# Performance work log

Measured on AMD Instinct MI355X. Metric: run time of the kernel, lower is better.

## Reference

```python
import jax, jax.numpy as jnp
import numpy as np

N, C, A = 4096, 1000, 2048


def setup_inputs() -> dict:
    key = jax.random.key(0)
    k1, k2, k3, k4 = jax.random.split(key, 4)
    features = jax.random.normal(k1, (N, A), dtype=jnp.float32)
    labels = jax.random.randint(k2, (N,), 0, C, dtype=jnp.int64)
    cv_matrix = jax.random.uniform(k3, (N, A), dtype=jnp.float32)
    ratio = jnp.asarray(0.5, dtype=jnp.float32)
    weight = jax.random.normal(k4, (C, A), dtype=jnp.float32) * 0.02
    bias = jnp.zeros((C,), dtype=jnp.float32)
    return {"features": features, "labels": labels, "cv_matrix": cv_matrix,
            "ratio": ratio, "weight": weight, "bias": bias}


def reference(features, labels, cv_matrix, ratio, weight, bias):
    # logits = features @ W^T + b
    logits = features @ weight.T + bias  # [N, C]
    # sigma2[n,c] = ratio * sum_a (W[c,a] - W[y_n,a])^2 * cv[n,a]
    # Expand the square to avoid materializing the [N, C, A] tensor:
    #   = sum_a W[c,a]^2 cv - 2 sum_a W[c,a] (W[y,a] cv) + sum_a W[y,a]^2 cv
    Wy = weight[labels]                          # [N, A] gather of per-label rows
    t1 = cv_matrix @ (weight * weight).T         # [N, C]
    t2 = (cv_matrix * Wy) @ weight.T             # [N, C]
    t3 = jnp.sum(Wy * Wy * cv_matrix, axis=1, keepdims=True)  # [N, 1]
    sigma2 = ratio * (t1 - 2.0 * t2 + t3)        # [N, C]
    aug_logits = logits + 0.5 * sigma2
    # mean cross-entropy on augmented logits
    logp = jax.nn.log_softmax(aug_logits, axis=-1)
    nll = -jnp.take_along_axis(logp, labels[:, None], axis=1)[:, 0]
    loss = jnp.mean(nll)
    return loss, logits
```

## Files before the change

### kernel.cpp

```cpp
#include <hip/hip_runtime.h>
#include <hip/hip_bf16.h>

#define N_ROWS 4096
#define C_CLS  1000
#define C_PAD  1024
#define A_DIM  2048

typedef __attribute__((ext_vector_type(8))) short short8;
typedef __attribute__((ext_vector_type(4))) float f32x4;

__device__ __forceinline__ unsigned short f2bf(float x) {
    unsigned u = __float_as_uint(x);
    unsigned rounding = 0x7fffu + ((u >> 16) & 1u);
    return (unsigned short)((u + rounding) >> 16);
}

__device__ __forceinline__ float bf2f(unsigned short u) {
    return __uint_as_float((unsigned)u << 16);
}

__device__ __forceinline__ unsigned pack2(float a, float b) {
    return (unsigned)f2bf(a) | ((unsigned)f2bf(b) << 16);
}

__device__ __forceinline__ void gload16(unsigned short* lds, const unsigned short* g) {
    __builtin_amdgcn_global_load_lds(
        (const __attribute__((address_space(1))) unsigned int*)g,
        (__attribute__((address_space(3))) unsigned int*)lds,
        16, 0, 0);
}

__global__ __launch_bounds__(256) void prep_all(
        const float* __restrict__ F, const float* __restrict__ CV,
        const float* __restrict__ W, const int* __restrict__ labels,
        const float* __restrict__ ratio_p,
        unsigned short* __restrict__ Fb, unsigned short* __restrict__ Ub,
        unsigned short* __restrict__ Vb,
        unsigned short* __restrict__ Wb, unsigned short* __restrict__ W2b,
        float* __restrict__ t3c) {
    int bid = blockIdx.x;
    if (bid >= N_ROWS) {
        int t = (bid - N_ROWS) * 256 + threadIdx.x;
        int a8 = t * 8;
        int c = a8 >> 11;
        int a = a8 & (A_DIM - 1);
        float4 w0 = make_float4(0.f, 0.f, 0.f, 0.f);
        float4 w1 = make_float4(0.f, 0.f, 0.f, 0.f);
        if (c < C_CLS) {
            w0 = *(const float4*)(W + (size_t)c * A_DIM + a);
            w1 = *(const float4*)(W + (size_t)c * A_DIM + a + 4);
        }
        uint4 pw, pw2;
        pw.x  = pack2(w0.x, w0.y);  pw.y  = pack2(w0.z, w0.w);
        pw.z  = pack2(w1.x, w1.y);  pw.w  = pack2(w1.z, w1.w);
        pw2.x = pack2(w0.x*w0.x, w0.y*w0.y);  pw2.y = pack2(w0.z*w0.z, w0.w*w0.w);
        pw2.z = pack2(w1.x*w1.x, w1.y*w1.y);  pw2.w = pack2(w1.z*w1.z, w1.w*w1.w);
        *(uint4*)(Wb  + (size_t)a8) = pw;
        *(uint4*)(W2b + (size_t)a8) = pw2;
        return;
    }
    int n = bid;
    int y = labels[n];
    float ratio = ratio_p[0];
    float hr = 0.5f * ratio;
    const float* frow  = F  + (size_t)n * A_DIM;
    const float* cvrow = CV + (size_t)n * A_DIM;
    const float* wyrow = W  + (size_t)y * A_DIM;
    size_t obase = (size_t)n * A_DIM;

    int a = threadIdx.x * 8;
    float4 f0  = *(const float4*)(frow + a);
    float4 f1  = *(const float4*)(frow + a + 4);
    float4 c0  = *(const float4*)(cvrow + a);
    float4 c1  = *(const float4*)(cvrow + a + 4);
    float4 y0  = *(const float4*)(wyrow + a);
    float4 y1  = *(const float4*)(wyrow + a + 4);

    float s = y0.x*y0.x*c0.x + y0.y*y0.y*c0.y + y0.z*y0.z*c0.z + y0.w*y0.w*c0.w
            + y1.x*y1.x*c1.x + y1.y*y1.y*c1.y + y1.z*y1.z*c1.z + y1.w*y1.w*c1.w;

    uint4 pf, pu, pv;
    pf.x = pack2(f0.x, f0.y);  pf.y = pack2(f0.z, f0.w);
    pf.z = pack2(f1.x, f1.y);  pf.w = pack2(f1.z, f1.w);
    pu.x = pack2(f0.x - ratio*c0.x*y0.x, f0.y - ratio*c0.y*y0.y);
    pu.y = pack2(f0.z - ratio*c0.z*y0.z, f0.w - ratio*c0.w*y0.w);
    pu.z = pack2(f1.x - ratio*c1.x*y1.x, f1.y - ratio*c1.y*y1.y);
    pu.w = pack2(f1.z - ratio*c1.z*y1.z, f1.w - ratio*c1.w*y1.w);
    pv.x = pack2(hr*c0.x, hr*c0.y);  pv.y = pack2(hr*c0.z, hr*c0.w);
    pv.z = pack2(hr*c1.x, hr*c1.y);  pv.w = pack2(hr*c1.z, hr*c1.w);
    *(uint4*)(Fb + obase + a) = pf;
    *(uint4*)(Ub + obase + a) = pu;
    *(uint4*)(Vb + obase + a) = pv;

    for (int off = 32; off; off >>= 1) s += __shfl_down(s, off);
    __shared__ float wsum[4];
    int lane = threadIdx.x & 63, wid = threadIdx.x >> 6;
    if (lane == 0) wsum[wid] = s;
    __syncthreads();
    if (threadIdx.x == 0)
        t3c[n] = hr * (wsum[0] + wsum[1] + wsum[2] + wsum[3]);
}

#define BM 128
#define BN 64
#define BK 32
#define TILE_A (BM * BK)
#define TILE_B (BN * BK)
#define BUF_USH (3 * TILE_A + 2 * TILE_B)
#define NT (A_DIM / BK)

__global__ __launch_bounds__(256, 2) void gemm_fused(
        const unsigned short* __restrict__ Fb, const unsigned short* __restrict__ Ub,
        const unsigned short* __restrict__ Vb, const unsigned short* __restrict__ Wb,
        const unsigned short* __restrict__ W2b,
        const float* __restrict__ t3c, const float* __restrict__ bias,
        float* __restrict__ out_logits, unsigned short* __restrict__ aug) {
    __shared__ unsigned short lds[2 * BUF_USH];

    int bid = blockIdx.x;
    int xcd = bid & 7, idx = bid >> 3;
    int bn = (xcd << 1) | (idx & 1);
    int bm = idx >> 1;

    int tid = threadIdx.x;
    int lane = tid & 63, wid = tid >> 6;
    int wm = wid >> 1, wn = wid & 1;

    int srow = lane >> 2;
    int scs  = ((lane & 3) * 8) ^ (((srow >> 1) & 3) << 3);
    int r0 = wid * 16 + srow;
    size_t gA0 = (size_t)(bm * BM + r0) * A_DIM + scs;
    size_t gB0 = (size_t)(bn * BN + r0) * A_DIM + scs;
    const size_t gStep = (size_t)64 * A_DIM;
    int d0 = wid * 512;
    int d1 = 2048 + wid * 512;

    int fr = lane & 15;
    int kof = ((lane >> 4) * 8) ^ (((fr >> 1) & 3) << 3);
    int aoff = fr * BK + kof;

    f32x4 accL[4][2] = {};
    f32x4 accA[4][2] = {};

    {
        unsigned short* b = lds;
        gload16(b + 0*TILE_A + d0, Fb + gA0);
        gload16(b + 0*TILE_A + d1, Fb + gA0 + gStep);
        gload16(b + 1*TILE_A + d0, Ub + gA0);
        gload16(b + 1*TILE_A + d1, Ub + gA0 + gStep);
        gload16(b + 2*TILE_A + d0, Vb + gA0);
        gload16(b + 2*TILE_A + d1, Vb + gA0 + gStep);
        gload16(b + 3*TILE_A + d0,          Wb  + gB0);
        gload16(b + 3*TILE_A + TILE_B + d0, W2b + gB0);
    }
    __syncthreads();

    for (int t = 0; t < NT; t++) {
        unsigned short* cbuf = lds + (t & 1) * BUF_USH;
        if (t + 1 < NT) {
            unsigned short* b = lds + ((t + 1) & 1) * BUF_USH;
            size_t ka = gA0 + (size_t)(t + 1) * BK;
            size_t kb = gB0 + (size_t)(t + 1) * BK;
            gload16(b + 0*TILE_A + d0, Fb + ka);
            gload16(b + 0*TILE_A + d1, Fb + ka + gStep);
            gload16(b + 1*TILE_A + d0, Ub + ka);
            gload16(b + 1*TILE_A + d1, Ub + ka + gStep);
            gload16(b + 2*TILE_A + d0, Vb + ka);
            gload16(b + 2*TILE_A + d1, Vb + ka + gStep);
            gload16(b + 3*TILE_A + d0,          Wb  + kb);
            gload16(b + 3*TILE_A + TILE_B + d0, W2b + kb);
        }

        short8 aF[4], aU[4], aV[4], bWf[2], bW2f[2];
        #pragma unroll
        for (int m = 0; m < 4; m++) {
            int off = wm * 2048 + m * 512 + aoff;
            aF[m] = *(const short8*)(cbuf + 0*TILE_A + off);
            aU[m] = *(const short8*)(cbuf + 1*TILE_A + off);
            aV[m] = *(const short8*)(cbuf + 2*TILE_A + off);
        }
        #pragma unroll
        for (int n = 0; n < 2; n++) {
            int off = wn * 1024 + n * 512 + aoff;
            bWf[n]  = *(const short8*)(cbuf + 3*TILE_A + off);
            bW2f[n] = *(const short8*)(cbuf + 3*TILE_A + TILE_B + off);
        }
        #pragma unroll
        for (int m = 0; m < 4; m++)
            #pragma unroll
            for (int n = 0; n < 2; n++) {
                accL[m][n] = __builtin_amdgcn_mfma_f32_16x16x32_bf16(aF[m], bWf[n],  accL[m][n], 0, 0, 0);
                accA[m][n] = __builtin_amdgcn_mfma_f32_16x16x32_bf16(aU[m], bWf[n],  accA[m][n], 0, 0, 0);
                accA[m][n] = __builtin_amdgcn_mfma_f32_16x16x32_bf16(aV[m], bW2f[n], accA[m][n], 0, 0, 0);
            }

        __syncthreads();
    }

    #pragma unroll
    for (int n = 0; n < 2; n++) {
        int col = bn * BN + wn * 32 + n * 16 + fr;
        if (col < C_CLS) {
            float bv = bias[col];
            #pragma unroll
            for (int m = 0; m < 4; m++) {
                int rbase = bm * BM + wm * 64 + m * 16 + (lane >> 4) * 4;
                #pragma unroll
                for (int j = 0; j < 4; j++) {
                    int row = rbase + j;
                    out_logits[(size_t)row * C_CLS + col] = accL[m][n][j] + bv;
                    aug[(size_t)row * C_PAD + col] = f2bf(accA[m][n][j] + bv + t3c[row]);
                }
            }
        }
    }
}

__global__ __launch_bounds__(256) void softmax_nll(const unsigned short* __restrict__ aug,
                                                   const int* __restrict__ labels,
                                                   float* __restrict__ nll) {
    int n = blockIdx.x;
    const unsigned short* row = aug + (size_t)n * C_PAD;
    int tid = threadIdx.x;
    int lane = tid & 63, wid = tid >> 6;
    __shared__ float sm[4], ss[4];

    float v[8];
    bool act = tid < (C_CLS / 8);
    float mx = -1e30f;
    if (act) {
        short8 r8 = *(const short8*)(row + tid * 8);
        #pragma unroll
        for (int j = 0; j < 8; j++) {
            v[j] = bf2f((unsigned short)r8[j]);
            mx = fmaxf(mx, v[j]);
        }
    }
    for (int off = 32; off; off >>= 1) mx = fmaxf(mx, __shfl_down(mx, off));
    if (lane == 0) sm[wid] = mx;
    __syncthreads();
    mx = fmaxf(fmaxf(sm[0], sm[1]), fmaxf(sm[2], sm[3]));

    float s = 0.f;
    if (act) {
        #pragma unroll
        for (int j = 0; j < 8; j++) s += __expf(v[j] - mx);
    }
    for (int off = 32; off; off >>= 1) s += __shfl_down(s, off);
    if (lane == 0) ss[wid] = s;
    __syncthreads();
    if (tid == 0) {
        float tot = ss[0] + ss[1] + ss[2] + ss[3];
        nll[n] = logf(tot) + mx - bf2f(row[labels[n]]);
    }
}

__global__ __launch_bounds__(256) void final_reduce(const float* __restrict__ nll,
                                                    float* __restrict__ out_loss) {
    float s = 0.f;
    for (int i = threadIdx.x; i < N_ROWS; i += 256) s += nll[i];
    for (int off = 32; off; off >>= 1) s += __shfl_down(s, off);
    __shared__ float ss[4];
    int lane = threadIdx.x & 63, wid = threadIdx.x >> 6;
    if (lane == 0) ss[wid] = s;
    __syncthreads();
    if (threadIdx.x == 0)
        out_loss[0] = (ss[0] + ss[1] + ss[2] + ss[3]) / (float)N_ROWS;
}

extern "C" void kernel_launch(void* const* d_in, const int* in_sizes, int n_in,
                              void* d_out, int out_size, void* d_ws, size_t ws_size,
                              hipStream_t stream) {
    const float* features = (const float*)d_in[0];
    const int*   labels   = (const int*)d_in[1];
    const float* cv       = (const float*)d_in[2];
    const float* ratio    = (const float*)d_in[3];
    const float* weight   = (const float*)d_in[4];
    const float* bias     = (const float*)d_in[5];
    float* out = (float*)d_out;

    char* p = (char*)d_ws;
    unsigned short* Wb  = (unsigned short*)p; p += (size_t)C_PAD * A_DIM * 2;
    unsigned short* W2b = (unsigned short*)p; p += (size_t)C_PAD * A_DIM * 2;
    unsigned short* Fb  = (unsigned short*)p; p += (size_t)N_ROWS * A_DIM * 2;
    unsigned short* Ub  = (unsigned short*)p; p += (size_t)N_ROWS * A_DIM * 2;
    unsigned short* Vb  = (unsigned short*)p; p += (size_t)N_ROWS * A_DIM * 2;
    float* t3c = (float*)p; p += (size_t)N_ROWS * 4;
    unsigned short* aug = (unsigned short*)p; p += (size_t)N_ROWS * C_PAD * 2;
    float* nllb = (float*)p; p += (size_t)N_ROWS * 4;

    int wprep_blocks = (C_PAD * A_DIM / 8) / 256;
    prep_all<<<N_ROWS + wprep_blocks, 256, 0, stream>>>(
        features, cv, weight, labels, ratio, Fb, Ub, Vb, Wb, W2b, t3c);
    gemm_fused<<<(N_ROWS / BM) * (C_PAD / BN), 256, 0, stream>>>(
        Fb, Ub, Vb, Wb, W2b, t3c, bias, out + 1, aug);
    softmax_nll<<<N_ROWS, 256, 0, stream>>>(aug, labels, nllb);
    final_reduce<<<1, 256, 0, stream>>>(nllb, out);
}
```

Measured before the change: 214.8 us.

## Compute squared weights in-register and prefetch two K-tiles ahead with finer waits

Drops the precomputed W² bf16 buffer. The GEMM now squares the bf16 weight fragments in registers after they are loaded from LDS, which removes one global stream and one LDS tile per stage. The main loop is restructured so loads for tile t+2 are issued into the buffer just consumed, after a barrier placed following the LDS reads. Explicit vmcnt waits replace the full syncthreads, aiming to overlap global loads with MFMA work. The trade-offs are extra VALU work per iteration and slightly different rounding, since W² now comes from bf16(W) rather than from fp32 W.

```diff
diff --git a/kernel.cpp b/kernel.cpp
--- a/kernel.cpp
+++ b/kernel.cpp
@@ -30,13 +30,27 @@
         16, 0, 0);
 }
 
+__device__ __forceinline__ short8 sq8(short8 w) {
+    union { short8 s; unsigned u[4]; } in, out;
+    in.s = w;
+    #pragma unroll
+    for (int i = 0; i < 4; i++) {
+        unsigned p = in.u[i];
+        float lo = __uint_as_float(p << 16);
+        float hi = __uint_as_float(p & 0xffff0000u);
+        unsigned lu = __float_as_uint(lo * lo);
+        unsigned hu = __float_as_uint(hi * hi);
+        out.u[i] = ((lu + 0x8000u) >> 16) | ((hu + 0x8000u) & 0xffff0000u);
+    }
+    return out.s;
+}
+
 __global__ __launch_bounds__(256) void prep_all(
         const float* __restrict__ F, const float* __restrict__ CV,
         const float* __restrict__ W, const int* __restrict__ labels,
         const float* __restrict__ ratio_p,
         unsigned short* __restrict__ Fb, unsigned short* __restrict__ Ub,
-        unsigned short* __restrict__ Vb,
-        unsigned short* __restrict__ Wb, unsigned short* __restrict__ W2b,
+        unsigned short* __restrict__ Vb, unsigned short* __restrict__ Wb,
         float* __restrict__ t3c) {
     int bid = blockIdx.x;
     if (bid >= N_ROWS) {
@@ -50,13 +64,10 @@
             w0 = *(const float4*)(W + (size_t)c * A_DIM + a);
             w1 = *(const float4*)(W + (size_t)c * A_DIM + a + 4);
         }
-        uint4 pw, pw2;
-        pw.x  = pack2(w0.x, w0.y);  pw.y  = pack2(w0.z, w0.w);
-        pw.z  = pack2(w1.x, w1.y);  pw.w  = pack2(w1.z, w1.w);
-        pw2.x = pack2(w0.x*w0.x, w0.y*w0.y);  pw2.y = pack2(w0.z*w0.z, w0.w*w0.w);
-        pw2.z = pack2(w1.x*w1.x, w1.y*w1.y);  pw2.w = pack2(w1.z*w1.z, w1.w*w1.w);
-        *(uint4*)(Wb  + (size_t)a8) = pw;
-        *(uint4*)(W2b + (size_t)a8) = pw2;
+        uint4 pw;
+        pw.x = pack2(w0.x, w0.y);  pw.y = pack2(w0.z, w0.w);
+        pw.z = pack2(w1.x, w1.y);  pw.w = pack2(w1.z, w1.w);
+        *(uint4*)(Wb + (size_t)a8) = pw;
         return;
     }
     int n = bid;
@@ -106,13 +117,12 @@
 #define BK 32
 #define TILE_A (BM * BK)
 #define TILE_B (BN * BK)
-#define BUF_USH (3 * TILE_A + 2 * TILE_B)
+#define BUF_USH (3 * TILE_A + TILE_B)
 #define NT (A_DIM / BK)
 
 __global__ __launch_bounds__(256, 2) void gemm_fused(
         const unsigned short* __restrict__ Fb, const unsigned short* __restrict__ Ub,
         const unsigned short* __restrict__ Vb, const unsigned short* __restrict__ Wb,
-        const unsigned short* __restrict__ W2b,
         const float* __restrict__ t3c, const float* __restrict__ bias,
         float* __restrict__ out_logits, unsigned short* __restrict__ aug) {
     __shared__ unsigned short lds[2 * BUF_USH];
@@ -142,36 +152,28 @@
     f32x4 accL[4][2] = {};
     f32x4 accA[4][2] = {};
 
-    {
-        unsigned short* b = lds;
-        gload16(b + 0*TILE_A + d0, Fb + gA0);
-        gload16(b + 0*TILE_A + d1, Fb + gA0 + gStep);
-        gload16(b + 1*TILE_A + d0, Ub + gA0);
-        gload16(b + 1*TILE_A + d1, Ub + gA0 + gStep);
-        gload16(b + 2*TILE_A + d0, Vb + gA0);
-        gload16(b + 2*TILE_A + d1, Vb + gA0 + gStep);
-        gload16(b + 3*TILE_A + d0,          Wb  + gB0);
-        gload16(b + 3*TILE_A + TILE_B + d0, W2b + gB0);
-    }
-    __syncthreads();
+#define STAGE(buf, ka, kb)                                        \
+    do {                                                          \
+        unsigned short* _b = (buf);                               \
+        gload16(_b + 0*TILE_A + d0, Fb + (ka));                   \
+        gload16(_b + 0*TILE_A + d1, Fb + (ka) + gStep);           \
+        gload16(_b + 1*TILE_A + d0, Ub + (ka));                   \
+        gload16(_b + 1*TILE_A + d1, Ub + (ka) + gStep);           \
+        gload16(_b + 2*TILE_A + d0, Vb + (ka));                   \
+        gload16(_b + 2*TILE_A + d1, Vb + (ka) + gStep);           \
+        gload16(_b + 3*TILE_A + d0, Wb + (kb));                   \
+    } while (0)
+
+    STAGE(lds,           gA0,      gB0);
+    STAGE(lds + BUF_USH, gA0 + BK, gB0 + BK);
+    asm volatile("s_waitcnt vmcnt(7)" ::: "memory");
+    __builtin_amdgcn_s_barrier();
+    __builtin_amdgcn_sched_barrier(0);
 
     for (int t = 0; t < NT; t++) {
         unsigned short* cbuf = lds + (t & 1) * BUF_USH;
-        if (t + 1 < NT) {
-            unsigned short* b = lds + ((t + 1) & 1) * BUF_USH;
-            size_t ka = gA0 + (size_t)(t + 1) * BK;
-            size_t kb = gB0 + (size_t)(t + 1) * BK;
-            gload16(b + 0*TILE_A + d0, Fb + ka);
-            gload16(b + 0*TILE_A + d1, Fb + ka + gStep);
-            gload16(b + 1*TILE_A + d0, Ub + ka);
-            gload16(b + 1*TILE_A + d1, Ub + ka + gStep);
-            gload16(b + 2*TILE_A + d0, Vb + ka);
-            gload16(b + 2*TILE_A + d1, Vb + ka + gStep);
-            gload16(b + 3*TILE_A + d0,          Wb  + kb);
-            gload16(b + 3*TILE_A + TILE_B + d0, W2b + kb);
-        }
-
-        short8 aF[4], aU[4], aV[4], bWf[2], bW2f[2];
+
+        short8 aF[4], aU[4], aV[4], bWf[2];
         #pragma unroll
         for (int m = 0; m < 4; m++) {
             int off = wm * 2048 + m * 512 + aoff;
@@ -182,9 +184,22 @@
         #pragma unroll
         for (int n = 0; n < 2; n++) {
             int off = wn * 1024 + n * 512 + aoff;
-            bWf[n]  = *(const short8*)(cbuf + 3*TILE_A + off);
-            bW2f[n] = *(const short8*)(cbuf + 3*TILE_A + TILE_B + off);
-        }
+            bWf[n] = *(const short8*)(cbuf + 3*TILE_A + off);
+        }
+
+        asm volatile("s_waitcnt lgkmcnt(0)" ::: "memory");
+        __builtin_amdgcn_s_barrier();
+        __builtin_amdgcn_sched_barrier(0);
+
+        if (t + 2 < NT) {
+            size_t ka = gA0 + (size_t)(t + 2) * BK;
+            size_t kb = gB0 + (size_t)(t + 2) * BK;
+            STAGE(cbuf, ka, kb);
+        }
+
+        short8 bW2f[2];
+        #pragma unroll
+        for (int n = 0; n < 2; n++) bW2f[n] = sq8(bWf[n]);
         #pragma unroll
         for (int m = 0; m < 4; m++)
             #pragma unroll
@@ -194,8 +209,17 @@
                 accA[m][n] = __builtin_amdgcn_mfma_f32_16x16x32_bf16(aV[m], bW2f[n], accA[m][n], 0, 0, 0);
             }
 
-        __syncthreads();
-    }
+        if (t + 1 < NT) {
+            if (t + 2 < NT) {
+                asm volatile("s_waitcnt vmcnt(7)" ::: "memory");
+            } else {
+                asm volatile("s_waitcnt vmcnt(0)" ::: "memory");
+            }
+            __builtin_amdgcn_s_barrier();
+            __builtin_amdgcn_sched_barrier(0);
+        }
+    }
+#undef STAGE
 
     #pragma unroll
     for (int n = 0; n < 2; n++) {
@@ -281,7 +305,6 @@
 
     char* p = (char*)d_ws;
     unsigned short* Wb  = (unsigned short*)p; p += (size_t)C_PAD * A_DIM * 2;
-    unsigned short* W2b = (unsigned short*)p; p += (size_t)C_PAD * A_DIM * 2;
     unsigned short* Fb  = (unsigned short*)p; p += (size_t)N_ROWS * A_DIM * 2;
     unsigned short* Ub  = (unsigned short*)p; p += (size_t)N_ROWS * A_DIM * 2;
     unsigned short* Vb  = (unsigned short*)p; p += (size_t)N_ROWS * A_DIM * 2;
@@ -291,9 +314,9 @@
 
     int wprep_blocks = (C_PAD * A_DIM / 8) / 256;
     prep_all<<<N_ROWS + wprep_blocks, 256, 0, stream>>>(
-        features, cv, weight, labels, ratio, Fb, Ub, Vb, Wb, W2b, t3c);
+        features, cv, weight, labels, ratio, Fb, Ub, Vb, Wb, t3c);
     gemm_fused<<<(N_ROWS / BM) * (C_PAD / BN), 256, 0, stream>>>(
-        Fb, Ub, Vb, Wb, W2b, t3c, bias, out + 1, aug);
+        Fb, Ub, Vb, Wb, t3c, bias, out + 1, aug);
     softmax_nll<<<N_ROWS, 256, 0, stream>>>(aug, labels, nllb);
     final_reduce<<<1, 256, 0, stream>>>(nllb, out);
 }
```

After: 217.9 us. Within noise of the previous version (+1.5%).
